# Kernel optimization log

Hardware: AMD Instinct MI355X
Metric: run time of the kernel (lower is better)

## Reference

```python
import jax, jax.numpy as jnp
import numpy as np

NG = 100000   # number of g-side nodes
NS = 100000   # number of s-side nodes
E = 640000    # edges per direction
D = 128       # feature / embed dim


def setup_inputs() -> dict:
    key = jax.random.key(0)
    ks = jax.random.split(key, 16)
    inp = {
        'Xg_self':  jax.random.normal(ks[0], (NG, D), jnp.float32),
        'Xs_self':  jax.random.normal(ks[1], (NS, D), jnp.float32),
        'Xs_for_g': jax.random.normal(ks[2], (NS, D), jnp.float32),
        'Xg_for_s': jax.random.normal(ks[3], (NG, D), jnp.float32),
        # COO edge lists for the two bipartite sparse adjacencies
        'row_gs': jax.random.randint(ks[4], (E,), 0, NG, jnp.int32),
        'col_gs': jax.random.randint(ks[5], (E,), 0, NS, jnp.int32),
        'val_gs': jax.random.uniform(ks[6], (E,), jnp.float32),
        'row_sg': jax.random.randint(ks[7], (E,), 0, NS, jnp.int32),
        'col_sg': jax.random.randint(ks[8], (E,), 0, NG, jnp.int32),
        'val_sg': jax.random.uniform(ks[9], (E,), jnp.float32),
        # Linear weights (PyTorch layout: [out_features, in_features], no bias)
        'Wg_self':  jax.random.normal(ks[10], (D, D), jnp.float32) * 0.05,
        'Wg_neigh': jax.random.normal(ks[11], (D, D), jnp.float32) * 0.05,
        'Ws_self':  jax.random.normal(ks[12], (D, D), jnp.float32) * 0.05,
        'Ws_neigh': jax.random.normal(ks[13], (D, D), jnp.float32) * 0.05,
    }
    return inp


def reference(Xg_self, Xs_self, Xs_for_g, Xg_for_s,
              row_gs, col_gs, val_gs, row_sg, col_sg, val_sg,
              Wg_self, Wg_neigh, Ws_self, Ws_neigh):
    # SpMM: neigh_g = A_gs @ Xs_for_g  (Ng x Ns sparse times Ns x D dense)
    neigh_g = jax.ops.segment_sum(Xs_for_g[col_gs] * val_gs[:, None], row_gs,
                                  num_segments=NG)
    # SpMM: neigh_s = A_sg @ Xg_for_s
    neigh_s = jax.ops.segment_sum(Xg_for_s[col_sg] * val_sg[:, None], row_sg,
                                  num_segments=NS)
    out_g = jax.nn.relu(Xg_self @ Wg_self.T + neigh_g @ Wg_neigh.T)
    out_s = jax.nn.relu(Xs_self @ Ws_self.T + neigh_s @ Ws_neigh.T)
    return (out_g, out_s)
```

## Files before the change

### kernel.cpp

```cpp
#include <hip/hip_runtime.h>
#include <hip/hip_bf16.h>
#include <stdint.h>

typedef __attribute__((ext_vector_type(4))) float f32x4;
typedef __attribute__((ext_vector_type(8))) short bf16x8;

#define D 128
#define GLOBAL_AS __attribute__((address_space(1)))
#define LDS_AS __attribute__((address_space(3)))

__device__ inline short f2bf(float x) {
    __hip_bfloat16 h = __float2bfloat16(x);
    return __builtin_bit_cast(short, h);
}

__device__ inline bf16x8 pack8(f32x4 lo, f32x4 hi) {
    bf16x8 b;
    b[0] = f2bf(lo[0]); b[1] = f2bf(lo[1]); b[2] = f2bf(lo[2]); b[3] = f2bf(lo[3]);
    b[4] = f2bf(hi[0]); b[5] = f2bf(hi[1]); b[6] = f2bf(hi[2]); b[7] = f2bf(hi[3]);
    return b;
}

__device__ inline unsigned int pack2bf(float a, float b) {
    unsigned int ua = (unsigned int)(unsigned short)f2bf(a);
    unsigned int ub = (unsigned int)(unsigned short)f2bf(b);
    return ua | (ub << 16);
}


__global__ __launch_bounds__(256)
void prep_kernel(const float* __restrict__ Xa, const float* __restrict__ Xb,
                 unsigned short* __restrict__ x16a, unsigned short* __restrict__ x16b,
                 const float* __restrict__ Wg_self, const float* __restrict__ Wg_neigh,
                 const float* __restrict__ Ws_self, const float* __restrict__ Ws_neigh,
                 short* __restrict__ Wcat,
                 const int* __restrict__ rowA, int EA,
                 const int* __restrict__ rowB, int NGoff,
                 int* __restrict__ cnt,
                 int n8a, int n8b, int Etot)
{
    int t = blockIdx.x * 256 + threadIdx.x;
    if (t < n8a) {
        f32x4 lo = *reinterpret_cast<const f32x4*>(Xa + (size_t)t * 8);
        f32x4 hi = *reinterpret_cast<const f32x4*>(Xa + (size_t)t * 8 + 4);
        *reinterpret_cast<bf16x8*>(x16a + (size_t)t * 8) = pack8(lo, hi);
        return;
    }
    t -= n8a;
    if (t < n8b) {
        f32x4 lo = *reinterpret_cast<const f32x4*>(Xb + (size_t)t * 8);
        f32x4 hi = *reinterpret_cast<const f32x4*>(Xb + (size_t)t * 8 + 4);
        *reinterpret_cast<bf16x8*>(x16b + (size_t)t * 8) = pack8(lo, hi);
        return;
    }
    t -= n8b;
    if (t < 2 * 128 * 32) {
        int dir = t >> 12;
        int rem = t & 4095;
        int j = rem >> 5;
        int k = (rem & 31) * 8;
        const float* Wself  = dir ? Ws_self  : Wg_self;
        const float* Wneigh = dir ? Ws_neigh : Wg_neigh;
        const float* src = (k < 128) ? (Wself + j * D + k) : (Wneigh + j * D + (k - 128));
        f32x4 lo = *reinterpret_cast<const f32x4*>(src);
        f32x4 hi = *reinterpret_cast<const f32x4*>(src + 4);
        *reinterpret_cast<bf16x8*>(Wcat + (size_t)dir * 32768 + j * 256 + k) = pack8(lo, hi);
        return;
    }
    t -= 2 * 128 * 32;
    if (t < Etot) {
        int r = (t < EA) ? rowA[t] : (rowB[t - EA] + NGoff);
        atomicAdd(&cnt[r], 1);
    }
}


__global__ __launch_bounds__(256)
void scan1_kernel(const int* __restrict__ cnt, int* __restrict__ part,
                  int* __restrict__ blksums, int N)
{
    __shared__ int wsum[4];
    int t = threadIdx.x;
    int base = blockIdx.x * 1024 + t * 4;
    int v0 = base + 0 < N ? cnt[base + 0] : 0;
    int v1 = base + 1 < N ? cnt[base + 1] : 0;
    int v2 = base + 2 < N ? cnt[base + 2] : 0;
    int v3 = base + 3 < N ? cnt[base + 3] : 0;
    int s = v0 + v1 + v2 + v3;
    int lane = t & 63, w = t >> 6;
    int x = s;
#pragma unroll
    for (int off = 1; off < 64; off <<= 1) {
        int y = __shfl_up(x, off);
        if (lane >= off) x += y;
    }
    if (lane == 63) wsum[w] = x;
    __syncthreads();
    int woff = 0;
    for (int i = 0; i < w; ++i) woff += wsum[i];
    int incl = x + woff;
    int excl = incl - s;
    if (base + 0 < N) part[base + 0] = excl;
    if (base + 1 < N) part[base + 1] = excl + v0;
    if (base + 2 < N) part[base + 2] = excl + v0 + v1;
    if (base + 3 < N) part[base + 3] = excl + v0 + v1 + v2;
    if (t == 255) blksums[blockIdx.x] = incl;
}

__global__ __launch_bounds__(256)
void scan2_kernel(int* __restrict__ blksums, int nb)
{
    __shared__ int wsum[4];
    int t = threadIdx.x;
    int v = t < nb ? blksums[t] : 0;
    int lane = t & 63, w = t >> 6;
    int x = v;
#pragma unroll
    for (int off = 1; off < 64; off <<= 1) {
        int y = __shfl_up(x, off);
        if (lane >= off) x += y;
    }
    if (lane == 63) wsum[w] = x;
    __syncthreads();
    int woff = 0;
    for (int i = 0; i < w; ++i) woff += wsum[i];
    int excl = x + woff - v;
    if (t < nb) blksums[t] = excl;
}

__global__ __launch_bounds__(256)
void scan3_kernel(int* __restrict__ cursor, const int* __restrict__ blksums, int N)
{
    int i = blockIdx.x * 256 + threadIdx.x;
    if (i < N) cursor[i] += blksums[i >> 10];
}

__global__ __launch_bounds__(256)
void fill2_kernel(const int* __restrict__ rowA, const int* __restrict__ colA,
                  const float* __restrict__ valA, int EA,
                  const int* __restrict__ rowB, const int* __restrict__ colB,
                  const float* __restrict__ valB, int NGoff,
                  int* __restrict__ cursor, int2* __restrict__ pairs, int Etot)
{
    int e = blockIdx.x * 256 + threadIdx.x;
    if (e >= Etot) return;
    int r, c; float v;
    if (e < EA) { r = rowA[e]; c = colA[e]; v = valA[e]; }
    else { int e2 = e - EA; r = rowB[e2] + NGoff; c = colB[e2]; v = valB[e2]; }
    int p = atomicAdd(&cursor[r], 1);
    pairs[p] = make_int2(c, __float_as_int(v));
}

__global__ __launch_bounds__(256)
void gather_kernel(const unsigned short* __restrict__ X16_0,
                   const unsigned short* __restrict__ X16_1,
                   const int* __restrict__ cnt, const int* __restrict__ endpos,
                   const int2* __restrict__ pairs,
                   unsigned short* __restrict__ neigh16, int NG, int N)
{
    int wid = (blockIdx.x * 256 + threadIdx.x) >> 6;
    if (wid >= N) return;
    int lane = threadIdx.x & 63;
    const unsigned short* X16 = (wid < NG) ? X16_0 : X16_1;
    int n = __builtin_amdgcn_readfirstlane(cnt[wid]);
    int s = __builtin_amdgcn_readfirstlane(endpos[wid]) - n;
    float acc0 = 0.f, acc1 = 0.f;
#pragma unroll 1
    for (int j = 0; j < n; j += 8) {
        int2 p[8]; unsigned int x[8];
#pragma unroll
        for (int u = 0; u < 8; ++u) {
            int idx = (j + u < n) ? j + u : n - 1;
            p[u] = pairs[s + idx];
        }
#pragma unroll
        for (int u = 0; u < 8; ++u)
            x[u] = *reinterpret_cast<const unsigned int*>(X16 + (size_t)p[u].x * D + lane * 2);
#pragma unroll
        for (int u = 0; u < 8; ++u) {
            float v = (j + u < n) ? __int_as_float(p[u].y) : 0.f;
            acc0 += __uint_as_float(x[u] << 16) * v;
            acc1 += __uint_as_float(x[u] & 0xffff0000u) * v;
        }
    }
    ((unsigned int*)neigh16)[(size_t)wid * 64 + lane] = pack2bf(acc0, acc1);
}

__global__ __launch_bounds__(256)
void gemm16_kernel(const float* __restrict__ Xself0, const float* __restrict__ Xself1,
                   const unsigned short* __restrict__ neigh16,
                   float* __restrict__ out0, int n0,
                   float* __restrict__ out1, int n1,
                   const short* __restrict__ Wcat)
{
    __shared__ float A[32 * 128];
    const int ROWS = 32;
    int blocks0 = (n0 + ROWS - 1) / ROWS;

    const float* Xself; float* out; int nRows, r0base, csr0; const short* Wb;
    if ((int)blockIdx.x < blocks0) {
        Xself = Xself0; out = out0; nRows = n0;
        r0base = blockIdx.x * ROWS; csr0 = 0; Wb = Wcat;
    } else {
        Xself = Xself1; out = out1; nRows = n1;
        r0base = ((int)blockIdx.x - blocks0) * ROWS; csr0 = n0; Wb = Wcat + 32768;
    }

    const int tid = threadIdx.x, wave = tid >> 6, lane = tid & 63;
    const int l15 = lane & 15, lhi = lane >> 4;

#pragma unroll
    for (int i = 0; i < 8; i += 2) {
        int r = wave * 8 + i + (lane >> 5);
        int R = r0base + r; if (R > nRows - 1) R = nRows - 1;
        const float* g = Xself + (size_t)R * D + (((lane & 31) ^ (r & 7)) << 2);
        __builtin_amdgcn_global_load_lds((const GLOBAL_AS uint32_t*)g,
                                         (LDS_AS uint32_t*)(&A[(wave * 8 + i) * 128]),
                                         16, 0, 0);
    }

    bf16x8 bfrag[2][8];
#pragma unroll
    for (int nn = 0; nn < 2; ++nn) {
        int j = wave * 32 + nn * 16 + l15;
#pragma unroll
        for (int kb = 0; kb < 8; ++kb)
            bfrag[nn][kb] = *reinterpret_cast<const bf16x8*>(
                Wb + (size_t)j * 256 + kb * 32 + lhi * 8);
    }

    bf16x8 nfrag[2][4];
#pragma unroll
    for (int it = 0; it < 2; ++it) {
        int R = r0base + it * 16 + l15; if (R > nRows - 1) R = nRows - 1;
#pragma unroll
        for (int k4 = 0; k4 < 4; ++k4)
            nfrag[it][k4] = *reinterpret_cast<const bf16x8*>(
                neigh16 + (size_t)(csr0 + R) * D + k4 * 32 + lhi * 8);
    }

    asm volatile("s_waitcnt vmcnt(0)" ::: "memory");
    __syncthreads();

#pragma unroll
    for (int it = 0; it < 2; ++it) {
        int r = it * 16 + l15;
        int rx = r & 7;
        f32x4 acc0 = {0.f, 0.f, 0.f, 0.f};
        f32x4 acc1 = {0.f, 0.f, 0.f, 0.f};
#pragma unroll
        for (int kb = 0; kb < 8; ++kb) {
            bf16x8 af;
            if (kb < 4) {
                int c0 = kb * 8 + lhi * 2;
                f32x4 lo = *reinterpret_cast<const f32x4*>(&A[r * 128 + ((c0 ^ rx) << 2)]);
                f32x4 hi = *reinterpret_cast<const f32x4*>(&A[r * 128 + (((c0 + 1) ^ rx) << 2)]);
                af = pack8(lo, hi);
            } else {
                af = nfrag[it][kb - 4];
            }
            acc0 = __builtin_amdgcn_mfma_f32_16x16x32_bf16(af, bfrag[0][kb], acc0, 0, 0, 0);
            acc1 = __builtin_amdgcn_mfma_f32_16x16x32_bf16(af, bfrag[1][kb], acc1, 0, 0, 0);
        }
#pragma unroll
        for (int i2 = 0; i2 < 4; ++i2) {
            int rr = r0base + it * 16 + lhi * 4 + i2;
            if (rr < nRows) {
                float v0 = acc0[i2] > 0.f ? acc0[i2] : 0.f;
                float v1 = acc1[i2] > 0.f ? acc1[i2] : 0.f;
                out[(size_t)rr * D + wave * 32 + l15]      = v0;
                out[(size_t)rr * D + wave * 32 + 16 + l15] = v1;
            }
        }
    }
}


__global__ __launch_bounds__(256)
void scatter_edges(const float* __restrict__ X, const int* __restrict__ row,
                   const int* __restrict__ col, const float* __restrict__ val,
                   float* out, int nE)
{
    int t = blockIdx.x * 256 + threadIdx.x;
    int e = t >> 5;
    if (e >= nE) return;
    int l = t & 31;
    int r = row[e];
    int c = col[e];
    float v = val[e];
    f32x4 x = *reinterpret_cast<const f32x4*>(X + (size_t)c * D + l * 4);
    float* o = out + (size_t)r * D + l * 4;
    unsafeAtomicAdd(o + 0, x[0] * v);
    unsafeAtomicAdd(o + 1, x[1] * v);
    unsafeAtomicAdd(o + 2, x[2] * v);
    unsafeAtomicAdd(o + 3, x[3] * v);
}

__global__ __launch_bounds__(256)
void gemm_relu_fb(const float* __restrict__ Xself, const float* __restrict__ Neigh,
                  const float* __restrict__ Wself, const float* __restrict__ Wneigh,
                  float* __restrict__ out, int nRows)
{
    const int tid  = threadIdx.x;
    const int wave = tid >> 6;
    const int lane = tid & 63;
    const int l15  = lane & 15;
    const int lhi  = lane >> 4;

    bf16x8 bfrag[2][8];
#pragma unroll
    for (int n = 0; n < 2; ++n) {
        int j = wave * 32 + n * 16 + l15;
#pragma unroll
        for (int kb = 0; kb < 8; ++kb) {
            int k = kb * 32 + lhi * 8;
            const float* src = (kb < 4) ? (Wself + j * D + k)
                                        : (Wneigh + j * D + (k - 128));
            f32x4 lo = *reinterpret_cast<const f32x4*>(src);
            f32x4 hi = *reinterpret_cast<const f32x4*>(src + 4);
            bfrag[n][kb] = pack8(lo, hi);
        }
    }

    int r0base = blockIdx.x * 128;
#pragma unroll 1
    for (int it = 0; it < 8; ++it) {
        int r0 = r0base + it * 16;
        if (r0 >= nRows) break;
        const float* xrow = Xself + (size_t)(r0 + l15) * D;
        const float* nrow = Neigh + (size_t)(r0 + l15) * D;
        bf16x8 afrag[8];
#pragma unroll
        for (int kb = 0; kb < 8; ++kb) {
            const float* src = (kb < 4) ? (xrow + kb * 32 + lhi * 8)
                                        : (nrow + (kb - 4) * 32 + lhi * 8);
            f32x4 lo = *reinterpret_cast<const f32x4*>(src);
            f32x4 hi = *reinterpret_cast<const f32x4*>(src + 4);
            afrag[kb] = pack8(lo, hi);
        }
        asm volatile("s_waitcnt vmcnt(0)" ::: "memory");
        __syncthreads();

        f32x4 acc0 = {0.f, 0.f, 0.f, 0.f};
        f32x4 acc1 = {0.f, 0.f, 0.f, 0.f};
#pragma unroll
        for (int kb = 0; kb < 8; ++kb) {
            acc0 = __builtin_amdgcn_mfma_f32_16x16x32_bf16(afrag[kb], bfrag[0][kb], acc0, 0, 0, 0);
            acc1 = __builtin_amdgcn_mfma_f32_16x16x32_bf16(afrag[kb], bfrag[1][kb], acc1, 0, 0, 0);
        }
#pragma unroll
        for (int i = 0; i < 4; ++i) {
            int rr = r0 + lhi * 4 + i;
            if (rr < nRows) {
                float v0 = acc0[i] > 0.f ? acc0[i] : 0.f;
                float v1 = acc1[i] > 0.f ? acc1[i] : 0.f;
                out[(size_t)rr * D + wave * 32 + l15]      = v0;
                out[(size_t)rr * D + wave * 32 + 16 + l15] = v1;
            }
        }
    }
}


extern "C" void kernel_launch(void* const* d_in, const int* in_sizes, int n_in,
                              void* d_out, int out_size, void* d_ws, size_t ws_size,
                              hipStream_t stream)
{
    const float* Xg_self  = (const float*)d_in[0];
    const float* Xs_self  = (const float*)d_in[1];
    const float* Xs_for_g = (const float*)d_in[2];
    const float* Xg_for_s = (const float*)d_in[3];
    const int*   row_gs   = (const int*)d_in[4];
    const int*   col_gs   = (const int*)d_in[5];
    const float* val_gs   = (const float*)d_in[6];
    const int*   row_sg   = (const int*)d_in[7];
    const int*   col_sg   = (const int*)d_in[8];
    const float* val_sg   = (const float*)d_in[9];
    const float* Wg_self  = (const float*)d_in[10];
    const float* Wg_neigh = (const float*)d_in[11];
    const float* Ws_self  = (const float*)d_in[12];
    const float* Ws_neigh = (const float*)d_in[13];

    const int NG = in_sizes[0] / D;
    const int NS = in_sizes[1] / D;
    const int E1 = in_sizes[4];
    const int E2 = in_sizes[7];
    const int N  = NG + NS;
    const int Etot = E1 + E2;

    float* out_g = (float*)d_out;
    float* out_s = out_g + (size_t)NG * D;

    size_t off = 0;
    auto alloc = [&](size_t bytes) -> size_t {
        off = (off + 255) & ~(size_t)255;
        size_t o = off;
        off += bytes;
        return o;
    };
    size_t x16g_o   = alloc(sizeof(short) * (size_t)NG * D);
    size_t x16s_o   = alloc(sizeof(short) * (size_t)NS * D);
    size_t wcat_o   = alloc(sizeof(short) * 2 * 128 * 256);
    size_t cnt_o    = alloc(sizeof(int) * N);
    size_t cursor_o = alloc(sizeof(int) * N);
    size_t pairs_o  = alloc(sizeof(int2) * (size_t)Etot);
    size_t blk_o    = alloc(sizeof(int) * 1024);
    size_t neigh_o  = alloc(sizeof(short) * (size_t)N * D);
    size_t need_bytes = off;

    char* ws = (char*)d_ws;

    if (ws_size < need_bytes) {
        hipMemsetAsync(d_out, 0, (size_t)out_size * sizeof(float), stream);
        {
            long long threads = (long long)E1 * 32;
            scatter_edges<<<(int)((threads + 255) / 256), 256, 0, stream>>>(
                Xs_for_g, row_gs, col_gs, val_gs, out_g, E1);
        }
        {
            long long threads = (long long)E2 * 32;
            scatter_edges<<<(int)((threads + 255) / 256), 256, 0, stream>>>(
                Xg_for_s, row_sg, col_sg, val_sg, out_s, E2);
        }
        gemm_relu_fb<<<(NG + 127) / 128, 256, 0, stream>>>(Xg_self, out_g, Wg_self, Wg_neigh, out_g, NG);
        gemm_relu_fb<<<(NS + 127) / 128, 256, 0, stream>>>(Xs_self, out_s, Ws_self, Ws_neigh, out_s, NS);
        return;
    }

    unsigned short* x16g    = (unsigned short*)(ws + x16g_o);
    unsigned short* x16s    = (unsigned short*)(ws + x16s_o);
    short* wcat             = (short*)(ws + wcat_o);
    int* cnt                = (int*)(ws + cnt_o);
    int* cursor             = (int*)(ws + cursor_o);
    int2* pairs             = (int2*)(ws + pairs_o);
    int* blk                = (int*)(ws + blk_o);
    unsigned short* neigh16 = (unsigned short*)(ws + neigh_o);

    const int n8a = NG * D / 8, n8b = NS * D / 8;

    hipMemsetAsync(cnt, 0, sizeof(int) * N, stream);

    {
        long long tot = (long long)n8a + n8b + 2 * 128 * 32 + Etot;
        prep_kernel<<<(int)((tot + 255) / 256), 256, 0, stream>>>(
            Xs_for_g, Xg_for_s, x16g, x16s,
            Wg_self, Wg_neigh, Ws_self, Ws_neigh, wcat,
            row_gs, E1, row_sg, NG, cnt, n8a, n8b, Etot);
    }

    int nb = (N + 1023) / 1024;
    scan1_kernel<<<nb, 256, 0, stream>>>(cnt, cursor, blk, N);
    scan2_kernel<<<1, 256, 0, stream>>>(blk, nb);
    scan3_kernel<<<(N + 255) / 256, 256, 0, stream>>>(cursor, blk, N);
    fill2_kernel<<<(Etot + 255) / 256, 256, 0, stream>>>(
        row_gs, col_gs, val_gs, E1, row_sg, col_sg, val_sg, NG, cursor, pairs, Etot);

    gather_kernel<<<(int)(((long long)N * 64 + 255) / 256), 256, 0, stream>>>(
        x16g, x16s, cnt, cursor, pairs, neigh16, NG, N);

    int blocks0 = (NG + 31) / 32, blocks1 = (NS + 31) / 32;
    gemm16_kernel<<<blocks0 + blocks1, 256, 0, stream>>>(
        Xg_self, Xs_self, neigh16, out_g, NG, out_s, NS, wcat);
}
```

Measured before the change: 336.8 us.

## Build CSR with two-level bucket sort to localize scatter atomics

```diff
diff --git a/kernel.cpp b/kernel.cpp
--- a/kernel.cpp
+++ b/kernel.cpp
@@ -129,26 +129,47 @@
 }
 
 __global__ __launch_bounds__(256)
-void scan3_kernel(int* __restrict__ cursor, const int* __restrict__ blksums, int N)
+void scan3_kernel(int* __restrict__ cursor, const int* __restrict__ blksums, int N,
+                  int* __restrict__ bstart, int* __restrict__ bcur)
 {
     int i = blockIdx.x * 256 + threadIdx.x;
-    if (i < N) cursor[i] += blksums[i >> 10];
-}
-
-__global__ __launch_bounds__(256)
-void fill2_kernel(const int* __restrict__ rowA, const int* __restrict__ colA,
-                  const float* __restrict__ valA, int EA,
-                  const int* __restrict__ rowB, const int* __restrict__ colB,
-                  const float* __restrict__ valB, int NGoff,
-                  int* __restrict__ cursor, int2* __restrict__ pairs, int Etot)
+    if (i < N) {
+        int v = cursor[i] + blksums[i >> 10];
+        cursor[i] = v;
+        if ((i & 63) == 0) { bstart[i >> 6] = v; bcur[i >> 6] = v; }
+    }
+}
+
+__global__ __launch_bounds__(256)
+void fill2b_kernel(const int* __restrict__ rowA, const int* __restrict__ colA,
+                   const float* __restrict__ valA, int EA,
+                   const int* __restrict__ rowB, const int* __restrict__ colB,
+                   const float* __restrict__ valB, int NGoff,
+                   int* __restrict__ bcur, int2* __restrict__ tmp, int Etot)
 {
     int e = blockIdx.x * 256 + threadIdx.x;
     if (e >= Etot) return;
-    int r, c; float v;
-    if (e < EA) { r = rowA[e]; c = colA[e]; v = valA[e]; }
-    else { int e2 = e - EA; r = rowB[e2] + NGoff; c = colB[e2]; v = valB[e2]; }
-    int p = atomicAdd(&cursor[r], 1);
-    pairs[p] = make_int2(c, __float_as_int(v));
+    int gid, c; float v;
+    if (e < EA) { gid = rowA[e]; c = colA[e]; v = valA[e]; }
+    else { int e2 = e - EA; gid = rowB[e2] + NGoff; c = colB[e2]; v = valB[e2]; }
+    int b = gid >> 6;
+    int p = atomicAdd(&bcur[b], 1);
+    tmp[p] = make_int2(c | ((gid & 63) << 17), __float_as_int(v));
+}
+
+__global__ __launch_bounds__(256)
+void sortref_kernel(const int2* __restrict__ tmp, const int* __restrict__ bstart,
+                    int NB, int Etot, int* __restrict__ cursor, int2* __restrict__ pairs)
+{
+    int b = blockIdx.x;
+    int bs = bstart[b];
+    int be = (b + 1 < NB) ? bstart[b + 1] : Etot;
+    for (int k = bs + (int)threadIdx.x; k < be; k += 256) {
+        int2 rec = tmp[k];
+        int gid = (b << 6) | ((unsigned)rec.x >> 17);
+        int p = atomicAdd(&cursor[gid], 1);
+        pairs[p] = rec;
+    }
 }
 
 __global__ __launch_bounds__(256)
@@ -174,8 +195,10 @@
             p[u] = pairs[s + idx];
         }
 #pragma unroll
-        for (int u = 0; u < 8; ++u)
-            x[u] = *reinterpret_cast<const unsigned int*>(X16 + (size_t)p[u].x * D + lane * 2);
+        for (int u = 0; u < 8; ++u) {
+            int c = p[u].x & 0x1FFFF;
+            x[u] = *reinterpret_cast<const unsigned int*>(X16 + (size_t)c * D + lane * 2);
+        }
 #pragma unroll
         for (int u = 0; u < 8; ++u) {
             float v = (j + u < n) ? __int_as_float(p[u].y) : 0.f;
@@ -387,6 +410,7 @@
     const int E2 = in_sizes[7];
     const int N  = NG + NS;
     const int Etot = E1 + E2;
+    const int NB = (N + 63) / 64;
 
     float* out_g = (float*)d_out;
     float* out_s = out_g + (size_t)NG * D;
@@ -404,7 +428,10 @@
     size_t cnt_o    = alloc(sizeof(int) * N);
     size_t cursor_o = alloc(sizeof(int) * N);
     size_t pairs_o  = alloc(sizeof(int2) * (size_t)Etot);
+    size_t tmp_o    = alloc(sizeof(int2) * (size_t)Etot);
     size_t blk_o    = alloc(sizeof(int) * 1024);
+    size_t bstart_o = alloc(sizeof(int) * (NB + 1));
+    size_t bcur_o   = alloc(sizeof(int) * (NB + 1));
     size_t neigh_o  = alloc(sizeof(short) * (size_t)N * D);
     size_t need_bytes = off;
 
@@ -433,7 +460,10 @@
     int* cnt                = (int*)(ws + cnt_o);
     int* cursor             = (int*)(ws + cursor_o);
     int2* pairs             = (int2*)(ws + pairs_o);
+    int2* tmp               = (int2*)(ws + tmp_o);
     int* blk                = (int*)(ws + blk_o);
+    int* bstart             = (int*)(ws + bstart_o);
+    int* bcur               = (int*)(ws + bcur_o);
     unsigned short* neigh16 = (unsigned short*)(ws + neigh_o);
 
     const int n8a = NG * D / 8, n8b = NS * D / 8;
@@ -451,9 +481,12 @@
     int nb = (N + 1023) / 1024;
     scan1_kernel<<<nb, 256, 0, stream>>>(cnt, cursor, blk, N);
     scan2_kernel<<<1, 256, 0, stream>>>(blk, nb);
-    scan3_kernel<<<(N + 255) / 256, 256, 0, stream>>>(cursor, blk, N);
-    fill2_kernel<<<(Etot + 255) / 256, 256, 0, stream>>>(
-        row_gs, col_gs, val_gs, E1, row_sg, col_sg, val_sg, NG, cursor, pairs, Etot);
+    scan3_kernel<<<(N + 255) / 256, 256, 0, stream>>>(cursor, blk, N, bstart, bcur);
+
+    fill2b_kernel<<<(Etot + 255) / 256, 256, 0, stream>>>(
+        row_gs, col_gs, val_gs, E1, row_sg, col_sg, val_sg, NG, bcur, tmp, Etot);
+
+    sortref_kernel<<<NB, 256, 0, stream>>>(tmp, bstart, NB, Etot, cursor, pairs);
 
     gather_kernel<<<(int)(((long long)N * 64 + 255) / 256), 256, 0, stream>>>(
         x16g, x16s, cnt, cursor, pairs, neigh16, NG, N);
```

New measurement: 448.0 us. 1.33x slower.
